# Kernel optimization log

Hardware: AMD Instinct MI355X
Metric: run time of the kernel (lower is better)

The kernel has to match this reference:

```python
import jax, jax.numpy as jnp
import numpy as np

B, S, H = 1, 2048, 1024
E, F, K = 8, 3584, 2


def setup_inputs() -> dict:
    key = jax.random.key(0)
    ks = jax.random.split(key, 5)
    scale_h = 1.0 / np.sqrt(H)
    scale_f = 1.0 / np.sqrt(F)
    return {
        "hidden_states": jax.random.normal(ks[0], (B, S, H), dtype=jnp.float32),
        "gate_w": jax.random.normal(ks[1], (E, H), dtype=jnp.float32) * scale_h,
        "w1": jax.random.normal(ks[2], (E, F, H), dtype=jnp.float32) * scale_h,
        "w2": jax.random.normal(ks[3], (E, H, F), dtype=jnp.float32) * scale_f,
        "w3": jax.random.normal(ks[4], (E, F, H), dtype=jnp.float32) * scale_h,
    }


def reference(hidden_states, gate_w, w1, w2, w3):
    b, s, h = hidden_states.shape
    x = hidden_states.reshape(-1, h)                      # [T, H]
    T = x.shape[0]
    router_logits = x @ gate_w.T                          # [T, E]
    probs = jax.nn.softmax(router_logits.astype(jnp.float32), axis=-1)
    rw, sel = jax.lax.top_k(probs, K)                     # [T, K]
    rw = rw / jnp.sum(rw, axis=-1, keepdims=True)
    rw = rw.astype(x.dtype)
    # combine weights per (token, expert): scatter top-k routing weights
    combine = jnp.zeros((T, E), dtype=x.dtype).at[
        jnp.arange(T)[:, None], sel
    ].add(rw)                                             # [T, E]
    out = jnp.zeros_like(x)
    for e in range(E):  # small fixed expert count
        # SwiGLU expert FFN (F.linear: x @ W.T)
        hmid = jax.nn.silu(x @ w1[e].T) * (x @ w3[e].T)   # [T, F]
        out = out + combine[:, e:e + 1] * (hmid @ w2[e].T)
    return out.reshape(b, s, h), router_logits
```

## Files before the change

kernel.cpp:

```cpp
#include <hip/hip_runtime.h>
#include <hip/hip_bf16.h>
#include <math.h>

namespace {
constexpr int kT = 2048;
constexpr int kH = 1024;
constexpr int kE = 8;
constexpr int kF = 3584;
constexpr int kK = 2;

constexpr size_t OFF_CNT  = 0;
constexpr size_t OFF_LIST = 1024;
constexpr size_t OFF_RW   = OFF_LIST + sizeof(int) * kE * kT;
constexpr size_t OFF_HMID = 1u << 20;
constexpr size_t OFF_XB   = 32u << 20;
constexpr size_t SZ_XB    = (size_t)kT * kH * 2;
constexpr size_t SZ_W     = (size_t)kE * kF * kH * 2;
constexpr size_t OFF_W1B  = OFF_XB + SZ_XB;
constexpr size_t OFF_W3B  = OFF_W1B + SZ_W;
constexpr size_t OFF_W2B  = OFF_W3B + SZ_W;
constexpr size_t WS_NEED  = OFF_W2B + SZ_W;

constexpr long NX8  = (long)kT * kH / 8;
constexpr long NW8  = (long)kE * kF * kH / 8;
constexpr long TOT8 = NX8 + 3 * NW8;

typedef __attribute__((ext_vector_type(8))) short bf16x8;
typedef __attribute__((ext_vector_type(4))) float fx4;
}

__device__ __forceinline__ short f2bf_s(float f) {
  union { __hip_bfloat16 h; short s; } u;
  u.h = __float2bfloat16(f);
  return u.s;
}

__device__ __forceinline__ bf16x8 pack8(float4 a, float4 b) {
  bf16x8 r;
  r[0] = f2bf_s(a.x); r[1] = f2bf_s(a.y);
  r[2] = f2bf_s(a.z); r[3] = f2bf_s(a.w);
  r[4] = f2bf_s(b.x); r[5] = f2bf_s(b.y);
  r[6] = f2bf_s(b.z); r[7] = f2bf_s(b.w);
  return r;
}

__device__ __forceinline__ int swz(int row, int u) {
  return row * 64 + ((u ^ (row & 7)) << 3);
}

__device__ __forceinline__ void gload16(const void* g, void* l) {
  __builtin_amdgcn_global_load_lds(
      (const __attribute__((address_space(1))) void*)g,
      (__attribute__((address_space(3))) void*)l, 16, 0, 0);
}

__global__ __launch_bounds__(256) void cast_all_kernel(
    const float* __restrict__ x, const float* __restrict__ w1,
    const float* __restrict__ w3, const float* __restrict__ w2,
    unsigned short* __restrict__ dst) {
  long i = (long)blockIdx.x * blockDim.x + threadIdx.x;
  const long stride = (long)gridDim.x * blockDim.x;
  for (; i < TOT8; i += stride) {
    const float* s; long o;
    if (i < NX8)              { s = x;  o = i; }
    else if (i < NX8 + NW8)   { s = w1; o = i - NX8; }
    else if (i < NX8 + 2*NW8) { s = w3; o = i - NX8 - NW8; }
    else                      { s = w2; o = i - NX8 - 2*NW8; }
    const float4* sp = reinterpret_cast<const float4*>(s + o * 8);
    const float4 v0 = sp[0], v1 = sp[1];
    *reinterpret_cast<bf16x8*>(dst + i * 8) = pack8(v0, v1);
  }
}

__global__ __launch_bounds__(256) void router_kernel(
    const float* __restrict__ x, const float* __restrict__ gw,
    float* __restrict__ logits_out, int* __restrict__ cnt,
    int* __restrict__ list, float* __restrict__ rw) {
  const int t = blockIdx.x;
  const float* xt = x + (size_t)t * kH;
  __shared__ float lg[kE];
  const int wave = threadIdx.x >> 6;
  const int lane = threadIdx.x & 63;
  for (int e = wave; e < kE; e += 4) {
    const float* g = gw + (size_t)e * kH;
    float s = 0.f;
    for (int h = lane; h < kH; h += 64) s += xt[h] * g[h];
#pragma unroll
    for (int off = 32; off > 0; off >>= 1) s += __shfl_down(s, off, 64);
    if (lane == 0) lg[e] = s;
  }
  __syncthreads();
  if (threadIdx.x < kE) logits_out[(size_t)t * kE + threadIdx.x] = lg[threadIdx.x];
  if (threadIdx.x == 0) {
    float m = lg[0];
#pragma unroll
    for (int e = 1; e < kE; ++e) m = fmaxf(m, lg[e]);
    float p[kE];
#pragma unroll
    for (int e = 0; e < kE; ++e) p[e] = expf(lg[e] - m);
    int i0 = 0;
#pragma unroll
    for (int e = 1; e < kE; ++e) if (p[e] > p[i0]) i0 = e;
    int i1 = (i0 == 0) ? 1 : 0;
#pragma unroll
    for (int e = 0; e < kE; ++e)
      if (e != i0 && e != i1 && p[e] > p[i1]) i1 = e;
    const float w0 = p[i0], w1v = p[i1];
    const float inv = 1.f / (w0 + w1v);
    rw[t * kK + 0] = w0 * inv;
    rw[t * kK + 1] = w1v * inv;
    const int s0 = atomicAdd(&cnt[i0], 1);
    list[i0 * kT + s0] = t * kK + 0;
    const int s1 = atomicAdd(&cnt[i1], 1);
    list[i1 * kT + s1] = t * kK + 1;
  }
}


__global__ __launch_bounds__(256) void moe_mid_gl(
    const unsigned short* __restrict__ xb, const unsigned short* __restrict__ w1b,
    const unsigned short* __restrict__ w3b, const int* __restrict__ cnt,
    const int* __restrict__ list, unsigned short* __restrict__ hmid) {
  const int e = blockIdx.z;
  const int n = cnt[e];
  const int t0 = blockIdx.y * 128;
  if (t0 >= n) return;
  const int f0 = blockIdx.x * 64;

  __shared__ short As[2][128 * 64];
  __shared__ short B1s[2][64 * 64];
  __shared__ short B3s[2][64 * 64];
  __shared__ int ppid[128];
  __shared__ int ptok[128];

  const int tid = threadIdx.x;
  if (tid < 128) {
    const int idx = t0 + tid;
    const int pid = (idx < n) ? list[e * kT + idx] : -1;
    ppid[tid] = pid;
    ptok[tid] = (pid < 0) ? 0 : (pid >> 1);
  }
  __syncthreads();

  const unsigned short* w1e = w1b + (size_t)e * kF * kH;
  const unsigned short* w3e = w3b + (size_t)e * kF * kH;

  const unsigned short* a_src[4];
#pragma unroll
  for (int c = 0; c < 4; ++c) {
    const int flat = tid + 256 * c;
    const int row = flat >> 3, u = flat & 7;
    a_src[c] = xb + (size_t)ptok[row] * kH + ((u ^ (row & 7)) * 8);
  }
  const unsigned short* b1_src[2]; const unsigned short* b3_src[2];
#pragma unroll
  for (int c = 0; c < 2; ++c) {
    const int flat = tid + 256 * c;
    const int row = flat >> 3, u = flat & 7;
    const int co = (u ^ (row & 7)) * 8;
    b1_src[c] = w1e + (size_t)(f0 + row) * kH + co;
    b3_src[c] = w3e + (size_t)(f0 + row) * kH + co;
  }

  const int lane = tid & 63, wid = tid >> 6;
  const int wr = wid >> 1, wc = wid & 1;
  const int lr = lane & 15, lq = lane >> 4;

  fx4 acc1[4][2], acc3[4][2];
#pragma unroll
  for (int i = 0; i < 4; ++i)
#pragma unroll
    for (int j = 0; j < 2; ++j) { acc1[i][j] = (fx4)(0.f); acc3[i][j] = (fx4)(0.f); }

  auto STAGE = [&](int buf, int k0) {
#pragma unroll
    for (int c = 0; c < 4; ++c)
      gload16(a_src[c] + k0, &As[buf][(tid + 256 * c) * 8]);
#pragma unroll
    for (int c = 0; c < 2; ++c) {
      gload16(b1_src[c] + k0, &B1s[buf][(tid + 256 * c) * 8]);
      gload16(b3_src[c] + k0, &B3s[buf][(tid + 256 * c) * 8]);
    }
  };
  auto MFMA_PHASE = [&](int buf) {
    const short* Ab = As[buf]; const short* B1b = B1s[buf]; const short* B3b = B3s[buf];
    __builtin_amdgcn_s_setprio(1);
#pragma unroll
    for (int ks = 0; ks < 2; ++ks) {
      bf16x8 a[4], bb1[2], bb3[2];
#pragma unroll
      for (int mi = 0; mi < 4; ++mi)
        a[mi] = *reinterpret_cast<const bf16x8*>(&Ab[swz(wr * 64 + mi * 16 + lr, ks * 4 + lq)]);
#pragma unroll
      for (int ni = 0; ni < 2; ++ni) {
        bb1[ni] = *reinterpret_cast<const bf16x8*>(&B1b[swz(wc * 32 + ni * 16 + lr, ks * 4 + lq)]);
        bb3[ni] = *reinterpret_cast<const bf16x8*>(&B3b[swz(wc * 32 + ni * 16 + lr, ks * 4 + lq)]);
      }
#pragma unroll
      for (int mi = 0; mi < 4; ++mi)
#pragma unroll
        for (int ni = 0; ni < 2; ++ni) {
          acc1[mi][ni] = __builtin_amdgcn_mfma_f32_16x16x32_bf16(a[mi], bb1[ni], acc1[mi][ni], 0, 0, 0);
          acc3[mi][ni] = __builtin_amdgcn_mfma_f32_16x16x32_bf16(a[mi], bb3[ni], acc3[mi][ni], 0, 0, 0);
        }
    }
    __builtin_amdgcn_s_setprio(0);
  };

  constexpr int NIT = kH / 64;
  STAGE(0, 0);
  __syncthreads();
  for (int it = 0; it < NIT; ++it) {
    const int cur = it & 1;
    if (it + 1 < NIT) STAGE(cur ^ 1, (it + 1) * 64);
    MFMA_PHASE(cur);
    __syncthreads();
  }

#pragma unroll
  for (int mi = 0; mi < 4; ++mi)
#pragma unroll
    for (int i = 0; i < 4; ++i) {
      const int row = wr * 64 + mi * 16 + lq * 4 + i;
      const int pid = ppid[row];
      if (pid < 0) continue;
#pragma unroll
      for (int ni = 0; ni < 2; ++ni) {
        const int col = f0 + wc * 32 + ni * 16 + lr;
        const float s1 = acc1[mi][ni][i];
        const float s3 = acc3[mi][ni][i];
        const float h = s1 * s3 / (1.f + expf(-s1));
        hmid[(size_t)pid * kF + col] = (unsigned short)f2bf_s(h);
      }
    }
}

__global__ __launch_bounds__(256) void moe_out_gl(
    const unsigned short* __restrict__ hmid, const unsigned short* __restrict__ w2b,
    const int* __restrict__ cnt, const int* __restrict__ list,
    const float* __restrict__ rw, float* __restrict__ out) {
  const int e = blockIdx.z;
  const int n = cnt[e];
  const int p0 = blockIdx.y * 128;
  if (p0 >= n) return;
  const int h0 = blockIdx.x * 64;

  __shared__ short As[2][128 * 64];
  __shared__ short Bs[2][64 * 64];
  __shared__ int ppid[128];
  __shared__ int prow[128];

  const int tid = threadIdx.x;
  if (tid < 128) {
    const int idx = p0 + tid;
    const int pid = (idx < n) ? list[e * kT + idx] : -1;
    ppid[tid] = pid;
    prow[tid] = (pid < 0) ? 0 : pid;
  }
  __syncthreads();

  const unsigned short* w2e = w2b + (size_t)e * kH * kF;

  const unsigned short* a_src[4];
#pragma unroll
  for (int c = 0; c < 4; ++c) {
    const int flat = tid + 256 * c;
    const int row = flat >> 3, u = flat & 7;
    a_src[c] = hmid + (size_t)prow[row] * kF + ((u ^ (row & 7)) * 8);
  }
  const unsigned short* b_src[2];
#pragma unroll
  for (int c = 0; c < 2; ++c) {
    const int flat = tid + 256 * c;
    const int row = flat >> 3, u = flat & 7;
    b_src[c] = w2e + (size_t)(h0 + row) * kF + ((u ^ (row & 7)) * 8);
  }

  const int lane = tid & 63, wid = tid >> 6;
  const int wr = wid >> 1, wc = wid & 1;
  const int lr = lane & 15, lq = lane >> 4;

  fx4 acc[4][2];
#pragma unroll
  for (int i = 0; i < 4; ++i)
#pragma unroll
    for (int j = 0; j < 2; ++j) acc[i][j] = (fx4)(0.f);

  auto STAGE = [&](int buf, int k0) {
#pragma unroll
    for (int c = 0; c < 4; ++c)
      gload16(a_src[c] + k0, &As[buf][(tid + 256 * c) * 8]);
#pragma unroll
    for (int c = 0; c < 2; ++c)
      gload16(b_src[c] + k0, &Bs[buf][(tid + 256 * c) * 8]);
  };
  auto MFMA_PHASE = [&](int buf) {
    const short* Ab = As[buf]; const short* Bb = Bs[buf];
    __builtin_amdgcn_s_setprio(1);
#pragma unroll
    for (int ks = 0; ks < 2; ++ks) {
      bf16x8 a[4], b[2];
#pragma unroll
      for (int mi = 0; mi < 4; ++mi)
        a[mi] = *reinterpret_cast<const bf16x8*>(&Ab[swz(wr * 64 + mi * 16 + lr, ks * 4 + lq)]);
#pragma unroll
      for (int ni = 0; ni < 2; ++ni)
        b[ni] = *reinterpret_cast<const bf16x8*>(&Bb[swz(wc * 32 + ni * 16 + lr, ks * 4 + lq)]);
#pragma unroll
      for (int mi = 0; mi < 4; ++mi)
#pragma unroll
        for (int ni = 0; ni < 2; ++ni)
          acc[mi][ni] = __builtin_amdgcn_mfma_f32_16x16x32_bf16(a[mi], b[ni], acc[mi][ni], 0, 0, 0);
    }
    __builtin_amdgcn_s_setprio(0);
  };

  constexpr int NIT = kF / 64;
  STAGE(0, 0);
  __syncthreads();
  for (int it = 0; it < NIT; ++it) {
    const int cur = it & 1;
    if (it + 1 < NIT) STAGE(cur ^ 1, (it + 1) * 64);
    MFMA_PHASE(cur);
    __syncthreads();
  }

#pragma unroll
  for (int mi = 0; mi < 4; ++mi)
#pragma unroll
    for (int i = 0; i < 4; ++i) {
      const int row = wr * 64 + mi * 16 + lq * 4 + i;
      const int pid = ppid[row];
      if (pid < 0) continue;
      const int tok = pid >> 1;
      const float w = rw[pid];
      float* op = out + (size_t)tok * kH + h0 + wc * 32 + lr;
#pragma unroll
      for (int ni = 0; ni < 2; ++ni)
        atomicAdd(&op[ni * 16], w * acc[mi][ni][i]);
    }
}

struct StageM { float4 a[2][2], b1[2][2], b3[2][2]; };

__global__ __launch_bounds__(256) void moe_mid_mfma(
    const float* __restrict__ x, const float* __restrict__ w1,
    const float* __restrict__ w3, const int* __restrict__ cnt,
    const int* __restrict__ list, unsigned short* __restrict__ hmid) {
  const int e = blockIdx.z;
  const int n = cnt[e];
  const int t0 = blockIdx.y * 64;
  if (t0 >= n) return;
  const int f0 = blockIdx.x * 64;

  __shared__ short As[2][64 * 64];
  __shared__ short B1s[2][64 * 64];
  __shared__ short B3s[2][64 * 64];
  __shared__ int ppid[64];
  __shared__ int ptok[64];

  const int tid = threadIdx.x;
  if (tid < 64) {
    const int idx = t0 + tid;
    const int pid = (idx < n) ? list[e * kT + idx] : -1;
    ppid[tid] = pid;
    ptok[tid] = (pid < 0) ? 0 : (pid >> 1);
  }
  __syncthreads();

  const float* w1e = w1 + (size_t)e * kF * kH;
  const float* w3e = w3 + (size_t)e * kF * kH;

  const float* a_src[2]; const float* b1_src[2]; const float* b3_src[2];
  int sw_[2];
#pragma unroll
  for (int i = 0; i < 2; ++i) {
    const int flat = tid + 256 * i;
    const int row = flat >> 3, u = flat & 7;
    a_src[i]  = x + (size_t)ptok[row] * kH + u * 8;
    b1_src[i] = w1e + (size_t)(f0 + row) * kH + u * 8;
    b3_src[i] = w3e + (size_t)(f0 + row) * kH + u * 8;
    sw_[i] = swz(row, u);
  }

  const int lane = tid & 63, wid = tid >> 6;
  const int wr = wid >> 1, wc = wid & 1;
  const int lr = lane & 15, lq = lane >> 4;

  fx4 acc1[2][2], acc3[2][2];
#pragma unroll
  for (int i = 0; i < 2; ++i)
#pragma unroll
    for (int j = 0; j < 2; ++j) { acc1[i][j] = (fx4)(0.f); acc3[i][j] = (fx4)(0.f); }

  auto LOAD = [&](StageM& S, int k0) {
#pragma unroll
    for (int i = 0; i < 2; ++i) {
      S.a[i][0]  = *reinterpret_cast<const float4*>(a_src[i] + k0);
      S.a[i][1]  = *reinterpret_cast<const float4*>(a_src[i] + k0 + 4);
      S.b1[i][0] = *reinterpret_cast<const float4*>(b1_src[i] + k0);
      S.b1[i][1] = *reinterpret_cast<const float4*>(b1_src[i] + k0 + 4);
      S.b3[i][0] = *reinterpret_cast<const float4*>(b3_src[i] + k0);
      S.b3[i][1] = *reinterpret_cast<const float4*>(b3_src[i] + k0 + 4);
    }
  };
  auto STORE = [&](const StageM& S, int buf) {
#pragma unroll
    for (int i = 0; i < 2; ++i) {
      *reinterpret_cast<bf16x8*>(&As[buf][sw_[i]])  = pack8(S.a[i][0], S.a[i][1]);
      *reinterpret_cast<bf16x8*>(&B1s[buf][sw_[i]]) = pack8(S.b1[i][0], S.b1[i][1]);
      *reinterpret_cast<bf16x8*>(&B3s[buf][sw_[i]]) = pack8(S.b3[i][0], S.b3[i][1]);
    }
  };
  auto MFMA_PHASE = [&](int buf) {
    const short* Ab = As[buf]; const short* B1b = B1s[buf]; const short* B3b = B3s[buf];
    __builtin_amdgcn_s_setprio(1);
#pragma unroll
    for (int ks = 0; ks < 2; ++ks) {
      bf16x8 a[2], bb1[2], bb3[2];
#pragma unroll
      for (int mi = 0; mi < 2; ++mi)
        a[mi] = *reinterpret_cast<const bf16x8*>(&Ab[swz(wr * 32 + mi * 16 + lr, ks * 4 + lq)]);
#pragma unroll
      for (int ni = 0; ni < 2; ++ni) {
        bb1[ni] = *reinterpret_cast<const bf16x8*>(&B1b[swz(wc * 32 + ni * 16 + lr, ks * 4 + lq)]);
        bb3[ni] = *reinterpret_cast<const bf16x8*>(&B3b[swz(wc * 32 + ni * 16 + lr, ks * 4 + lq)]);
      }
#pragma unroll
      for (int mi = 0; mi < 2; ++mi)
#pragma unroll
        for (int ni = 0; ni < 2; ++ni) {
          acc1[mi][ni] = __builtin_amdgcn_mfma_f32_16x16x32_bf16(a[mi], bb1[ni], acc1[mi][ni], 0, 0, 0);
          acc3[mi][ni] = __builtin_amdgcn_mfma_f32_16x16x32_bf16(a[mi], bb3[ni], acc3[mi][ni], 0, 0, 0);
        }
    }
    __builtin_amdgcn_s_setprio(0);
  };

  StageM R0, R1;
  constexpr int NIT = kH / 64;
  LOAD(R0, 0);
  LOAD(R1, 64);
  STORE(R0, 0);
  __syncthreads();
#pragma unroll 2
  for (int it = 0; it < NIT; ++it) {
    if (it & 1) {
      if (it + 2 < NIT) LOAD(R1, (it + 2) * 64);
      MFMA_PHASE(1);
      if (it + 1 < NIT) STORE(R0, 0);
    } else {
      if (it + 2 < NIT) LOAD(R0, (it + 2) * 64);
      MFMA_PHASE(0);
      if (it + 1 < NIT) STORE(R1, 1);
    }
    __syncthreads();
  }

#pragma unroll
  for (int mi = 0; mi < 2; ++mi)
#pragma unroll
    for (int i = 0; i < 4; ++i) {
      const int row = wr * 32 + mi * 16 + lq * 4 + i;
      const int pid = ppid[row];
      if (pid < 0) continue;
#pragma unroll
      for (int ni = 0; ni < 2; ++ni) {
        const int col = f0 + wc * 32 + ni * 16 + lr;
        const float s1 = acc1[mi][ni][i];
        const float s3 = acc3[mi][ni][i];
        const float h = s1 * s3 / (1.f + expf(-s1));
        hmid[(size_t)pid * kF + col] = (unsigned short)f2bf_s(h);
      }
    }
}

struct StageO { bf16x8 a[2]; float4 b[2][2]; };

__global__ __launch_bounds__(256) void moe_out_mfma(
    const unsigned short* __restrict__ hmid, const float* __restrict__ w2,
    const int* __restrict__ cnt, const int* __restrict__ list,
    const float* __restrict__ rw, float* __restrict__ out) {
  const int e = blockIdx.z;
  const int n = cnt[e];
  const int p0 = blockIdx.y * 64;
  if (p0 >= n) return;
  const int h0 = blockIdx.x * 64;

  __shared__ short As[2][64 * 64];
  __shared__ short Bs[2][64 * 64];
  __shared__ int ppid[64];
  __shared__ int prow[64];

  const int tid = threadIdx.x;
  if (tid < 64) {
    const int idx = p0 + tid;
    const int pid = (idx < n) ? list[e * kT + idx] : -1;
    ppid[tid] = pid;
    prow[tid] = (pid < 0) ? 0 : pid;
  }
  __syncthreads();

  const float* w2e = w2 + (size_t)e * kH * kF;

  const unsigned short* a_src[2]; const float* b_src[2];
  int sw_[2];
#pragma unroll
  for (int i = 0; i < 2; ++i) {
    const int flat = tid + 256 * i;
    const int row = flat >> 3, u = flat & 7;
    a_src[i] = hmid + (size_t)prow[row] * kF + u * 8;
    b_src[i] = w2e + (size_t)(h0 + row) * kF + u * 8;
    sw_[i] = swz(row, u);
  }

  const int lane = tid & 63, wid = tid >> 6;
  const int wr = wid >> 1, wc = wid & 1;
  const int lr = lane & 15, lq = lane >> 4;

  fx4 acc[2][2];
#pragma unroll
  for (int i = 0; i < 2; ++i)
#pragma unroll
    for (int j = 0; j < 2; ++j) acc[i][j] = (fx4)(0.f);

  auto LOAD = [&](StageO& S, int k0) {
#pragma unroll
    for (int i = 0; i < 2; ++i) {
      S.a[i]    = *reinterpret_cast<const bf16x8*>(a_src[i] + k0);
      S.b[i][0] = *reinterpret_cast<const float4*>(b_src[i] + k0);
      S.b[i][1] = *reinterpret_cast<const float4*>(b_src[i] + k0 + 4);
    }
  };
  auto STORE = [&](const StageO& S, int buf) {
#pragma unroll
    for (int i = 0; i < 2; ++i) {
      *reinterpret_cast<bf16x8*>(&As[buf][sw_[i]]) = S.a[i];
      *reinterpret_cast<bf16x8*>(&Bs[buf][sw_[i]]) = pack8(S.b[i][0], S.b[i][1]);
    }
  };
  auto MFMA_PHASE = [&](int buf) {
    const short* Ab = As[buf]; const short* Bb = Bs[buf];
    __builtin_amdgcn_s_setprio(1);
#pragma unroll
    for (int ks = 0; ks < 2; ++ks) {
      bf16x8 a[2], b[2];
#pragma unroll
      for (int mi = 0; mi < 2; ++mi)
        a[mi] = *reinterpret_cast<const bf16x8*>(&Ab[swz(wr * 32 + mi * 16 + lr, ks * 4 + lq)]);
#pragma unroll
      for (int ni = 0; ni < 2; ++ni)
        b[ni] = *reinterpret_cast<const bf16x8*>(&Bb[swz(wc * 32 + ni * 16 + lr, ks * 4 + lq)]);
#pragma unroll
      for (int mi = 0; mi < 2; ++mi)
#pragma unroll
        for (int ni = 0; ni < 2; ++ni)
          acc[mi][ni] = __builtin_amdgcn_mfma_f32_16x16x32_bf16(a[mi], b[ni], acc[mi][ni], 0, 0, 0);
    }
    __builtin_amdgcn_s_setprio(0);
  };

  StageO R0, R1;
  constexpr int NIT = kF / 64;
  LOAD(R0, 0);
  LOAD(R1, 64);
  STORE(R0, 0);
  __syncthreads();
#pragma unroll 2
  for (int it = 0; it < NIT; ++it) {
    if (it & 1) {
      if (it + 2 < NIT) LOAD(R1, (it + 2) * 64);
      MFMA_PHASE(1);
      if (it + 1 < NIT) STORE(R0, 0);
    } else {
      if (it + 2 < NIT) LOAD(R0, (it + 2) * 64);
      MFMA_PHASE(0);
      if (it + 1 < NIT) STORE(R1, 1);
    }
    __syncthreads();
  }

#pragma unroll
  for (int mi = 0; mi < 2; ++mi)
#pragma unroll
    for (int i = 0; i < 4; ++i) {
      const int row = wr * 32 + mi * 16 + lq * 4 + i;
      const int pid = ppid[row];
      if (pid < 0) continue;
      const int tok = pid >> 1;
      const float w = rw[pid];
      float* op = out + (size_t)tok * kH + h0 + wc * 32 + lr;
#pragma unroll
      for (int ni = 0; ni < 2; ++ni)
        atomicAdd(&op[ni * 16], w * acc[mi][ni][i]);
    }
}

extern "C" void kernel_launch(void* const* d_in, const int* in_sizes, int n_in,
                              void* d_out, int out_size, void* d_ws,
                              size_t ws_size, hipStream_t stream) {
  (void)in_sizes; (void)n_in; (void)out_size;
  const float* x  = (const float*)d_in[0];
  const float* gw = (const float*)d_in[1];
  const float* w1 = (const float*)d_in[2];
  const float* w2 = (const float*)d_in[3];
  const float* w3 = (const float*)d_in[4];

  float* out    = (float*)d_out;
  float* logits = out + (size_t)kT * kH;

  char* ws = (char*)d_ws;
  int*            cnt  = (int*)(ws + OFF_CNT);
  int*            list = (int*)(ws + OFF_LIST);
  float*          rw   = (float*)(ws + OFF_RW);
  unsigned short* hmid = (unsigned short*)(ws + OFF_HMID);

  hipMemsetAsync(out, 0, (size_t)kT * kH * sizeof(float), stream);
  hipMemsetAsync(cnt, 0, kE * sizeof(int), stream);

  router_kernel<<<kT, 256, 0, stream>>>(x, gw, logits, cnt, list, rw);

  if (ws_size >= WS_NEED) {
    unsigned short* xb  = (unsigned short*)(ws + OFF_XB);
    unsigned short* w1b = (unsigned short*)(ws + OFF_W1B);
    unsigned short* w3b = (unsigned short*)(ws + OFF_W3B);
    unsigned short* w2b = (unsigned short*)(ws + OFF_W2B);

    cast_all_kernel<<<2048, 256, 0, stream>>>(x, w1, w3, w2, xb);

    dim3 g1(kF / 64, kT / 128, kE);
    moe_mid_gl<<<g1, 256, 0, stream>>>(xb, w1b, w3b, cnt, list, hmid);

    dim3 g2(kH / 64, kT / 128, kE);
    moe_out_gl<<<g2, 256, 0, stream>>>(hmid, w2b, cnt, list, rw, out);
  } else {
    dim3 g1(kF / 64, kT / 64, kE);
    moe_mid_mfma<<<g1, 256, 0, stream>>>(x, w1, w3, cnt, list, hmid);

    dim3 g2(kH / 64, kT / 64, kE);
    moe_out_mfma<<<g2, 256, 0, stream>>>(hmid, w2, cnt, list, rw, out);
  }
}
```

Measured before the change: 360.4 us.

## Deepen GEMM prefetch with explicit vmcnt waits and nontemporal cast loads

```diff
diff --git a/kernel.cpp b/kernel.cpp
--- a/kernel.cpp
+++ b/kernel.cpp
@@ -41,6 +41,15 @@
   r[2] = f2bf_s(a.z); r[3] = f2bf_s(a.w);
   r[4] = f2bf_s(b.x); r[5] = f2bf_s(b.y);
   r[6] = f2bf_s(b.z); r[7] = f2bf_s(b.w);
+  return r;
+}
+
+__device__ __forceinline__ bf16x8 pack8v(fx4 a, fx4 b) {
+  bf16x8 r;
+  r[0] = f2bf_s(a[0]); r[1] = f2bf_s(a[1]);
+  r[2] = f2bf_s(a[2]); r[3] = f2bf_s(a[3]);
+  r[4] = f2bf_s(b[0]); r[5] = f2bf_s(b[1]);
+  r[6] = f2bf_s(b[2]); r[7] = f2bf_s(b[3]);
   return r;
 }
 
@@ -66,9 +75,10 @@
     else if (i < NX8 + NW8)   { s = w1; o = i - NX8; }
     else if (i < NX8 + 2*NW8) { s = w3; o = i - NX8 - NW8; }
     else                      { s = w2; o = i - NX8 - 2*NW8; }
-    const float4* sp = reinterpret_cast<const float4*>(s + o * 8);
-    const float4 v0 = sp[0], v1 = sp[1];
-    *reinterpret_cast<bf16x8*>(dst + i * 8) = pack8(v0, v1);
+    const fx4* sp = reinterpret_cast<const fx4*>(s + o * 8);
+    const fx4 v0 = __builtin_nontemporal_load(sp);
+    const fx4 v1 = __builtin_nontemporal_load(sp + 1);
+    *reinterpret_cast<bf16x8*>(dst + i * 8) = pack8v(v0, v1);
   }
 }
 
@@ -209,12 +219,15 @@
 
   constexpr int NIT = kH / 64;
   STAGE(0, 0);
-  __syncthreads();
+  STAGE(1, 64);
   for (int it = 0; it < NIT; ++it) {
     const int cur = it & 1;
-    if (it + 1 < NIT) STAGE(cur ^ 1, (it + 1) * 64);
+    if (it + 1 < NIT) asm volatile("s_waitcnt vmcnt(8)" ::: "memory");
+    else              asm volatile("s_waitcnt vmcnt(0)" ::: "memory");
+    asm volatile("s_barrier" ::: "memory");
     MFMA_PHASE(cur);
-    __syncthreads();
+    asm volatile("s_barrier" ::: "memory");
+    if (it + 2 < NIT) STAGE(cur, (it + 2) * 64);
   }
 
 #pragma unroll
@@ -317,12 +330,15 @@
 
   constexpr int NIT = kF / 64;
   STAGE(0, 0);
-  __syncthreads();
+  STAGE(1, 64);
   for (int it = 0; it < NIT; ++it) {
     const int cur = it & 1;
-    if (it + 1 < NIT) STAGE(cur ^ 1, (it + 1) * 64);
+    if (it + 1 < NIT) asm volatile("s_waitcnt vmcnt(6)" ::: "memory");
+    else              asm volatile("s_waitcnt vmcnt(0)" ::: "memory");
+    asm volatile("s_barrier" ::: "memory");
     MFMA_PHASE(cur);
-    __syncthreads();
+    asm volatile("s_barrier" ::: "memory");
+    if (it + 2 < NIT) STAGE(cur, (it + 2) * 64);
   }
 
 #pragma unroll
```

New measurement: 317.2 us. 12.0% less time.
